# Optimization experiments

Hardware: AMD Instinct MI355X
Metric: run time of the kernel (lower is better)

## Reference

```python
import jax, jax.numpy as jnp
import numpy as np

NUM_BLOCKS = 2
NUM_LAYERS = 10
L = NUM_BLOCKS * NUM_LAYERS  # 20 wave layers
C_IN, C_RES, C_SKIP = 8, 64, 256
B, T = 32, 4096


def causal_conv1d(x, w, b, dilation=1):
    # x: [B, C_in, T], w: [C_out, C_in, K], left-pad so output is causal and length-preserving
    k = w.shape[2]
    out = jax.lax.conv_general_dilated(
        x, w, window_strides=(1,), padding=[(dilation * (k - 1), 0)],
        rhs_dilation=(dilation,), dimension_numbers=("NCH", "OIH", "NCH"))
    return out + b[None, :, None]


def setup_inputs() -> dict:
    key = jax.random.key(0)
    ks = jax.random.split(key, 12)
    s1 = 1.0 / np.sqrt(C_IN)
    s2 = 1.0 / np.sqrt(2 * C_RES)
    s3 = 1.0 / np.sqrt(C_RES)
    return {
        "x":    jax.random.normal(ks[0], (B, C_IN, T), jnp.float32),
        "w_in": jax.random.normal(ks[1], (C_RES, C_IN, 1), jnp.float32) * s1,
        "b_in": jax.random.normal(ks[2], (C_RES,), jnp.float32) * s1,
        "w_f":  jax.random.normal(ks[3], (L, C_RES, C_RES, 2), jnp.float32) * s2,
        "b_f":  jax.random.normal(ks[4], (L, C_RES), jnp.float32) * s2,
        "w_g":  jax.random.normal(ks[5], (L, C_RES, C_RES, 2), jnp.float32) * s2,
        "b_g":  jax.random.normal(ks[6], (L, C_RES), jnp.float32) * s2,
        "w_s":  jax.random.normal(ks[7], (L, C_SKIP, C_RES, 1), jnp.float32) * s3,
        "b_s":  jax.random.normal(ks[8], (L, C_SKIP), jnp.float32) * s3,
        "w_r":  jax.random.normal(ks[9], (L, C_RES, C_RES, 1), jnp.float32) * s3,
        "b_r":  jax.random.normal(ks[10], (L, C_RES), jnp.float32) * s3,
    }


def reference(x, w_in, b_in, w_f, b_f, w_g, b_g, w_s, b_s, w_r, b_r):
    # WaveNet.encode: 1x1 input conv, then num_blocks*num_layers gated dilated causal layers
    h = causal_conv1d(x, w_in, b_in)            # [B, C_RES, T]
    skips = jnp.zeros((x.shape[0], w_s.shape[1], x.shape[2]), x.dtype)
    for i in range(L):
        d = 2 ** (i % NUM_LAYERS)
        f = jnp.tanh(causal_conv1d(h, w_f[i], b_f[i], d))
        g = jax.nn.sigmoid(causal_conv1d(h, w_g[i], b_g[i], d))
        z = f * g                                # gated activation
        skips = skips + causal_conv1d(z, w_s[i], b_s[i])
        h = h + causal_conv1d(z, w_r[i], b_r[i])  # residual connection
    return skips
```

## Files before the change

### kernel.cpp

```cpp
#include <hip/hip_runtime.h>

#define B_ 32
#define T_ 4096
#define CR 64
#define CS 256
#define NL 20

typedef __bf16 bf16x8 __attribute__((ext_vector_type(8)));
typedef __bf16 bf16x4v __attribute__((ext_vector_type(4)));
typedef float f32x4 __attribute__((ext_vector_type(4)));

__device__ __forceinline__ f32x4 mfma16(bf16x8 a, bf16x8 b, f32x4 c) {
  return __builtin_amdgcn_mfma_f32_16x16x32_bf16(a, b, c, 0, 0, 0);
}

__global__ void pack_kernel(const float* __restrict__ wf, const float* __restrict__ wg,
                            const float* __restrict__ wsn, const float* __restrict__ wr,
                            const float* __restrict__ bs,
                            __bf16* __restrict__ Wfg2, __bf16* __restrict__ Wr2,
                            __bf16* __restrict__ Ws2, float* __restrict__ bsS) {
  int n = blockIdx.x * 256 + threadIdx.x;
  if (n < 327680) {
    int j = n & 7, lane = (n >> 3) & 63, fr = (n >> 9) & 7, mt = (n >> 12) & 3, i = n >> 14;
    int cs = mt * 16 + (lane & 15);
    int k = (fr & 3) * 32 + (lane >> 4) * 8 + j;
    int ci = k & 63, tap = k >> 6;
    const float* src = (fr < 4) ? wf : wg;
    Wfg2[n] = (__bf16)src[((i * 64 + cs) * 64 + ci) * 2 + tap];
  } else if (n < 409600) {
    int m = n - 327680;
    int j = m & 7, lane = (m >> 3) & 63, kc = (m >> 9) & 1, mt = (m >> 10) & 3, i = m >> 12;
    int cs = mt * 16 + (lane & 15);
    int ci = kc * 32 + (lane >> 4) * 8 + j;
    Wr2[m] = (__bf16)wr[(i * 64 + cs) * 64 + ci];
  } else if (n < 737280) {
    int m = n - 409600;
    int j = m & 7, lane = (m >> 3) & 63, kc = (m >> 9) & 1, tile = (m >> 10) & 15, i = m >> 14;
    int cs = tile * 16 + (lane & 15);
    int ci = kc * 32 + (lane >> 4) * 8 + j;
    Ws2[m] = (__bf16)wsn[i * 16384 + cs * 64 + ci];
  } else if (n < 737536) {
    int cs = n - 737280;
    float s = 0.f;
    for (int i = 0; i < NL; ++i) s += bs[i * 256 + cs];
    bsS[cs] = s;
  }
}

__global__ void inconv_kernel(const float* __restrict__ x, const float* __restrict__ w_in,
                              const float* __restrict__ b_in, float* __restrict__ h0) {
  __shared__ float w[64][8];
  __shared__ float bi[64];
  int tid = threadIdx.x;
  for (int k = tid; k < 512; k += 256) w[k >> 3][k & 7] = w_in[k];
  if (tid < 64) bi[tid] = b_in[tid];
  __syncthreads();
  int b = blockIdx.x >> 4;
  int t = ((blockIdx.x & 15) << 8) + tid;
  float xv[8];
#pragma unroll
  for (int ci = 0; ci < 8; ++ci) xv[ci] = x[((size_t)b * 8 + ci) * T_ + t];
  float* orow = h0 + ((size_t)b * T_ + t) * 64;
#pragma unroll
  for (int c0 = 0; c0 < 64; c0 += 4) {
    float s0 = bi[c0], s1 = bi[c0 + 1], s2 = bi[c0 + 2], s3 = bi[c0 + 3];
#pragma unroll
    for (int ci = 0; ci < 8; ++ci) {
      s0 += w[c0][ci] * xv[ci];
      s1 += w[c0 + 1][ci] * xv[ci];
      s2 += w[c0 + 2][ci] * xv[ci];
      s3 += w[c0 + 3][ci] * xv[ci];
    }
    float4 o = make_float4(s0, s1, s2, s3);
    *(float4*)(orow + c0) = o;
  }
}

__global__ __launch_bounds__(256) void layer_kernel(
    const float* __restrict__ h_in, float* __restrict__ h_out,
    const __bf16* __restrict__ Wfg, const __bf16* __restrict__ Wr,
    const float* __restrict__ bF, const float* __restrict__ bG,
    const float* __restrict__ bR,
    __bf16* __restrict__ Zg, int d, int il, int Gs) {
  __shared__ __bf16 sB[2][64][72];

  const int tid = threadIdx.x;
  const int bid = ((blockIdx.x & 7) << 8) | (blockIdx.x >> 3);
  const int b = bid >> 6;
  const int t0 = (bid & 63) << 6;
  const float* hbase = h_in + ((size_t)b * T_ + t0) * 64;

  float4 vc[4], vd[4];
#pragma unroll
  for (int it = 0; it < 4; ++it) {
    int f = (it * 256 + tid) * 4;
    int trr = f >> 6, c = f & 63;
    vc[it] = *(const float4*)(hbase + trr * 64 + c);
    int td = t0 + trr - d;
    vd[it] = make_float4(0.f, 0.f, 0.f, 0.f);
    if (td >= 0) vd[it] = *(const float4*)(h_in + ((size_t)b * T_ + td) * 64 + c);
  }
#pragma unroll
  for (int it = 0; it < 4; ++it) {
    int f = (it * 256 + tid) * 4;
    int trr = f >> 6, c = f & 63;
    bf16x4v pc = {(__bf16)vc[it].x, (__bf16)vc[it].y, (__bf16)vc[it].z, (__bf16)vc[it].w};
    *(bf16x4v*)&sB[1][trr][c] = pc;
    bf16x4v pd = {(__bf16)vd[it].x, (__bf16)vd[it].y, (__bf16)vd[it].z, (__bf16)vd[it].w};
    *(bf16x4v*)&sB[0][trr][c] = pd;
  }
  __syncthreads();

  const int lane = tid & 63, wid = tid >> 6;
  const int tl = (wid << 4) | (lane & 15);
  const int kq = lane >> 4;

  bf16x8 bh[4];
  bh[0] = *(const bf16x8*)&sB[0][tl][kq * 8];
  bh[1] = *(const bf16x8*)&sB[0][tl][32 + kq * 8];
  bh[2] = *(const bf16x8*)&sB[1][tl][kq * 8];
  bh[3] = *(const bf16x8*)&sB[1][tl][32 + kq * 8];

  __bf16 (*sZ)[72] = sB[0];
  __bf16* zrow = Zg + (((size_t)b * T_ + t0 + tl) * Gs + il) * 64;

#pragma unroll
  for (int mt = 0; mt < 4; ++mt) {
    const __bf16* wb = Wfg + (mt * 8) * 512 + lane * 8;
    f32x4 aF = {0.f, 0.f, 0.f, 0.f}, aG = {0.f, 0.f, 0.f, 0.f};
#pragma unroll
    for (int kc = 0; kc < 4; ++kc) {
      aF = mfma16(*(const bf16x8*)(wb + kc * 512), bh[kc], aF);
      aG = mfma16(*(const bf16x8*)(wb + (4 + kc) * 512), bh[kc], aG);
    }
    const int c0 = (mt << 4) + (kq << 2);
    float4 bfv = *(const float4*)(bF + c0);
    float4 bgv = *(const float4*)(bG + c0);
    float fb[4] = {bfv.x, bfv.y, bfv.z, bfv.w};
    float gb[4] = {bgv.x, bgv.y, bgv.z, bgv.w};
    bf16x4v zv;
#pragma unroll
    for (int r = 0; r < 4; ++r) {
      float fp = aF[r] + fb[r];
      float gp = aG[r] + gb[r];
      float e = __expf(2.f * fp);
      float th = 1.f - 2.f / (e + 1.f);
      float sg = 1.f / (1.f + __expf(-gp));
      zv[r] = (__bf16)(th * sg);
    }
    *(bf16x4v*)&sZ[tl][c0] = zv;
    *(bf16x4v*)(zrow + c0) = zv;
  }

  bf16x8 bz0 = *(const bf16x8*)&sZ[tl][kq * 8];
  bf16x8 bz1 = *(const bf16x8*)&sZ[tl][32 + kq * 8];
#pragma unroll
  for (int mt = 0; mt < 4; ++mt) {
    const __bf16* wrb = Wr + (mt * 2) * 512 + lane * 8;
    f32x4 aR = {0.f, 0.f, 0.f, 0.f};
    aR = mfma16(*(const bf16x8*)(wrb), bz0, aR);
    aR = mfma16(*(const bf16x8*)(wrb + 512), bz1, aR);
    const int c0 = (mt << 4) + (kq << 2);
    float4 hv = *(const float4*)(h_in + ((size_t)b * T_ + t0 + tl) * 64 + c0);
    float4 brv = *(const float4*)(bR + c0);
    float4 o;
    o.x = hv.x + aR[0] + brv.x;
    o.y = hv.y + aR[1] + brv.y;
    o.z = hv.z + aR[2] + brv.z;
    o.w = hv.w + aR[3] + brv.w;
    *(float4*)(h_out + ((size_t)b * T_ + t0 + tl) * 64 + c0) = o;
  }
}

__global__ __launch_bounds__(256) void skip_kernel(
    const __bf16* __restrict__ Zg, const __bf16* __restrict__ Ws2,
    const float* __restrict__ bsS, float* __restrict__ out,
    int i0, int cnt, int Gs, int first) {
  __shared__ __bf16 sZ[2][64][72];

  const int tid = threadIdx.x;
  const int b = blockIdx.x >> 6;
  const int t0 = (blockIdx.x & 63) << 6;
  const int lane = tid & 63, wid = tid >> 6;
  const int kq = lane >> 4;
  const int tr = tid >> 2, coff = (tid & 3) << 4;

  const __bf16* zbase = Zg + (((size_t)b * T_ + t0 + tr) * Gs) * 64 + coff;
  const __bf16* wbase = Ws2 + (size_t)i0 * 16384 + (size_t)(wid * 8) * 512 + lane * 8;

  uint4 a0 = *(const uint4*)zbase;
  uint4 a1 = *(const uint4*)(zbase + 8);
  bf16x8 aw[8];
#pragma unroll
  for (int f = 0; f < 8; ++f) aw[f] = *(const bf16x8*)(wbase + f * 512);
  uint4 p0 = {0, 0, 0, 0}, p1 = {0, 0, 0, 0};
  if (cnt > 1) {
    p0 = *(const uint4*)(zbase + 64);
    p1 = *(const uint4*)(zbase + 72);
  }
  *(uint4*)&sZ[0][tr][coff] = a0;
  *(uint4*)&sZ[0][tr][coff + 8] = a1;

  f32x4 acc[16];
#pragma unroll
  for (int q = 0; q < 16; ++q) acc[q] = (f32x4){0.f, 0.f, 0.f, 0.f};

  asm volatile("s_waitcnt lgkmcnt(0)" ::: "memory");
  __builtin_amdgcn_sched_barrier(0);
  __builtin_amdgcn_s_barrier();
  __builtin_amdgcn_sched_barrier(0);

  const char* zrow0 = (const char*)&sZ[0][0][0] + (lane & 15) * 144 + kq * 16;

  for (int il = 0; il < cnt; ++il) {
    const int cur = il & 1;
    const bool have1 = (il + 1) < cnt;
    const bool have2 = (il + 2) < cnt;

    bf16x8 awn[8];
    if (have1) {
#pragma unroll
      for (int f = 0; f < 8; ++f)
        awn[f] = *(const bf16x8*)(wbase + (size_t)(il + 1) * 16384 + f * 512);
    }
    uint4 q0, q1;
    if (have2) {
      q0 = *(const uint4*)(zbase + (size_t)(il + 2) * 64);
      q1 = *(const uint4*)(zbase + (size_t)(il + 2) * 64 + 8);
    }

    bf16x8 bz[8];
#pragma unroll
    for (int nt = 0; nt < 4; ++nt) {
      bz[nt * 2]     = *(const bf16x8*)(zrow0 + cur * 9216 + nt * 2304);
      bz[nt * 2 + 1] = *(const bf16x8*)(zrow0 + cur * 9216 + nt * 2304 + 64);
    }
#pragma unroll
    for (int mt = 0; mt < 4; ++mt) {
#pragma unroll
      for (int nt = 0; nt < 4; ++nt) {
        acc[mt * 4 + nt] = mfma16(aw[mt * 2], bz[nt * 2], acc[mt * 4 + nt]);
        acc[mt * 4 + nt] = mfma16(aw[mt * 2 + 1], bz[nt * 2 + 1], acc[mt * 4 + nt]);
      }
    }

    if (have1) {
      *(uint4*)&sZ[cur ^ 1][tr][coff] = p0;
      *(uint4*)&sZ[cur ^ 1][tr][coff + 8] = p1;
      if (have2) { p0 = q0; p1 = q1; }
#pragma unroll
      for (int f = 0; f < 8; ++f) aw[f] = awn[f];
      asm volatile("s_waitcnt lgkmcnt(0)" ::: "memory");
      __builtin_amdgcn_sched_barrier(0);
      __builtin_amdgcn_s_barrier();
      __builtin_amdgcn_sched_barrier(0);
    }
  }

  const int csb = wid * 64 + (kq << 2);
  const int tcol = t0 + (lane & 15);
#pragma unroll
  for (int mt = 0; mt < 4; ++mt) {
#pragma unroll
    for (int nt = 0; nt < 4; ++nt) {
#pragma unroll
      for (int r = 0; r < 4; ++r) {
        int cs = csb + mt * 16 + r;
        size_t idx = ((size_t)b * CS + cs) * T_ + tcol + nt * 16;
        float v = acc[mt * 4 + nt][r];
        if (first) out[idx] = v + bsS[cs];
        else out[idx] += v;
      }
    }
  }
}

extern "C" void kernel_launch(void* const* d_in, const int* in_sizes, int n_in,
                              void* d_out, int out_size, void* d_ws, size_t ws_size,
                              hipStream_t stream) {
  (void)in_sizes; (void)n_in; (void)out_size;
  const float* x    = (const float*)d_in[0];
  const float* w_in = (const float*)d_in[1];
  const float* b_in = (const float*)d_in[2];
  const float* w_f  = (const float*)d_in[3];
  const float* b_f  = (const float*)d_in[4];
  const float* w_g  = (const float*)d_in[5];
  const float* b_g  = (const float*)d_in[6];
  const float* w_s  = (const float*)d_in[7];
  const float* b_s  = (const float*)d_in[8];
  const float* w_r  = (const float*)d_in[9];
  const float* b_r  = (const float*)d_in[10];
  float* out = (float*)d_out;

  char* ws = (char*)d_ws;
  size_t off = 0;
  auto alloc = [&](size_t bytes) -> char* {
    char* p = ws + off;
    off = (off + bytes + 255) & ~(size_t)255;
    return p;
  };
  float* hA = (float*)alloc((size_t)B_ * T_ * 64 * 4);
  float* hB = (float*)alloc((size_t)B_ * T_ * 64 * 4);
  __bf16* Wfg2 = (__bf16*)alloc((size_t)NL * 16384 * 2);
  __bf16* Wr2  = (__bf16*)alloc((size_t)NL * 4096 * 2);
  __bf16* Ws2  = (__bf16*)alloc((size_t)NL * 16384 * 2);
  float* bsS = (float*)alloc(CS * 4);

  size_t zslot = (size_t)B_ * T_ * 64 * 2;
  size_t rem = (ws_size > off) ? (ws_size - off) : 0;
  int G = (int)(rem / zslot);
  if (G > NL) G = NL;
  if (G < 1) G = 1;
  __bf16* Zg = (__bf16*)(ws + off);

  hipLaunchKernelGGL(pack_kernel, dim3(2881), dim3(256), 0, stream,
                     w_f, w_g, w_s, w_r, b_s, Wfg2, Wr2, Ws2, bsS);
  hipLaunchKernelGGL(inconv_kernel, dim3(512), dim3(256), 0, stream, x, w_in, b_in, hA);

  float* hc = hA;
  float* hn = hB;
  int i0 = 0;
  for (int i = 0; i < NL; ++i) {
    int il = i - i0;
    hipLaunchKernelGGL(layer_kernel, dim3(B_ * 64), dim3(256), 0, stream,
                       hc, hn, Wfg2 + (size_t)i * 16384, Wr2 + (size_t)i * 4096,
                       b_f + i * 64, b_g + i * 64, b_r + i * 64,
                       Zg, 1 << (i % 10), il, G);
    { float* tmp = hc; hc = hn; hn = tmp; }
    if (il + 1 == G || i == NL - 1) {
      int cnt = il + 1;
      hipLaunchKernelGGL(skip_kernel, dim3(B_ * 64), dim3(256), 0, stream,
                         Zg, Ws2, bsS, out, i0, cnt, G, (i0 == 0) ? 1 : 0);
      i0 = i + 1;
    }
  }
}
```

Before: 1.011 ms.

## Store Z in MFMA-fragment tile layout and DMA it into LDS with triple buffering

The layer kernel now writes gated activations Z into per-block 4096-element tiles already arranged in MFMA B-fragment order, replacing row-major rows. The skip kernel loads these tiles with global_load_lds (direct global-to-LDS DMA) into a three-slot LDS ring two iterations ahead, and ping-pongs weight registers between awA and awB so no register copy is needed. LDS reads become contiguous lane*8 fragment loads with no padding. The aim is to remove the register-staged LDS stores and the waits on them, at the cost of hand-tuned vmcnt counts that must match the issued loads exactly.

```diff
diff --git a/kernel.cpp b/kernel.cpp
--- a/kernel.cpp
+++ b/kernel.cpp
@@ -12,6 +12,12 @@
 
 __device__ __forceinline__ f32x4 mfma16(bf16x8 a, bf16x8 b, f32x4 c) {
   return __builtin_amdgcn_mfma_f32_16x16x32_bf16(a, b, c, 0, 0, 0);
+}
+
+__device__ __forceinline__ void dma16(const __bf16* g, __bf16* l) {
+  __builtin_amdgcn_global_load_lds(
+      (const __attribute__((address_space(1))) unsigned int*)g,
+      (__attribute__((address_space(3))) unsigned int*)l, 16, 0, 0);
 }
 
 __global__ void pack_kernel(const float* __restrict__ wf, const float* __restrict__ wg,
@@ -122,7 +128,7 @@
   bh[3] = *(const bf16x8*)&sB[1][tl][32 + kq * 8];
 
   __bf16 (*sZ)[72] = sB[0];
-  __bf16* zrow = Zg + (((size_t)b * T_ + t0 + tl) * Gs + il) * 64;
+  __bf16* ztile = Zg + ((size_t)bid * Gs + il) * 4096;
 
 #pragma unroll
   for (int mt = 0; mt < 4; ++mt) {
@@ -149,7 +155,12 @@
       zv[r] = (__bf16)(th * sg);
     }
     *(bf16x4v*)&sZ[tl][c0] = zv;
-    *(bf16x4v*)(zrow + c0) = zv;
+    {
+      const int kc = mt >> 1;
+      const int l = ((mt & 1) * 2 + (kq >> 1)) * 16 + (lane & 15);
+      const int j0 = (kq & 1) * 4;
+      *(bf16x4v*)(ztile + (size_t)(wid * 2 + kc) * 512 + l * 8 + j0) = zv;
+    }
   }
 
   bf16x8 bz0 = *(const bf16x8*)&sZ[tl][kq * 8];
@@ -176,85 +187,95 @@
     const __bf16* __restrict__ Zg, const __bf16* __restrict__ Ws2,
     const float* __restrict__ bsS, float* __restrict__ out,
     int i0, int cnt, int Gs, int first) {
-  __shared__ __bf16 sZ[2][64][72];
+  __shared__ __bf16 sZ[3][4096];
 
   const int tid = threadIdx.x;
   const int b = blockIdx.x >> 6;
   const int t0 = (blockIdx.x & 63) << 6;
   const int lane = tid & 63, wid = tid >> 6;
   const int kq = lane >> 4;
-  const int tr = tid >> 2, coff = (tid & 3) << 4;
-
-  const __bf16* zbase = Zg + (((size_t)b * T_ + t0 + tr) * Gs) * 64 + coff;
+
+  const __bf16* ztile = Zg + ((size_t)blockIdx.x * Gs + i0) * 4096;
   const __bf16* wbase = Ws2 + (size_t)i0 * 16384 + (size_t)(wid * 8) * 512 + lane * 8;
-
-  uint4 a0 = *(const uint4*)zbase;
-  uint4 a1 = *(const uint4*)(zbase + 8);
-  bf16x8 aw[8];
-#pragma unroll
-  for (int f = 0; f < 8; ++f) aw[f] = *(const bf16x8*)(wbase + f * 512);
-  uint4 p0 = {0, 0, 0, 0}, p1 = {0, 0, 0, 0};
+  __bf16* ldsw = &sZ[0][0] + (size_t)(wid * 2) * 512;
+
+#define DMA_TILE(ilx, bufx)                                                   \
+  do {                                                                        \
+    const __bf16* gsrc_ = ztile + (size_t)(ilx) * 4096 + (wid * 2) * 512 + lane * 8; \
+    __bf16* ld_ = ldsw + (size_t)(bufx) * 4096;                               \
+    dma16(gsrc_, ld_);                                                        \
+    dma16(gsrc_ + 512, ld_ + 512);                                            \
+  } while (0)
+
+  f32x4 acc[16];
+#pragma unroll
+  for (int q = 0; q < 16; ++q) acc[q] = (f32x4){0.f, 0.f, 0.f, 0.f};
+
+  bf16x8 awA[8], awB[8];
+
+  DMA_TILE(0, 0);
+  __builtin_amdgcn_sched_barrier(0);
+#pragma unroll
+  for (int f = 0; f < 8; ++f) awA[f] = *(const bf16x8*)(wbase + f * 512);
+  __builtin_amdgcn_sched_barrier(0);
   if (cnt > 1) {
-    p0 = *(const uint4*)(zbase + 64);
-    p1 = *(const uint4*)(zbase + 72);
-  }
-  *(uint4*)&sZ[0][tr][coff] = a0;
-  *(uint4*)&sZ[0][tr][coff + 8] = a1;
-
-  f32x4 acc[16];
-#pragma unroll
-  for (int q = 0; q < 16; ++q) acc[q] = (f32x4){0.f, 0.f, 0.f, 0.f};
-
-  asm volatile("s_waitcnt lgkmcnt(0)" ::: "memory");
-  __builtin_amdgcn_sched_barrier(0);
+    DMA_TILE(1, 1);
+    __builtin_amdgcn_sched_barrier(0);
+    asm volatile("s_waitcnt vmcnt(10)" ::: "memory");
+  } else {
+    __builtin_amdgcn_sched_barrier(0);
+    asm volatile("s_waitcnt vmcnt(8)" ::: "memory");
+  }
   __builtin_amdgcn_s_barrier();
   __builtin_amdgcn_sched_barrier(0);
 
-  const char* zrow0 = (const char*)&sZ[0][0][0] + (lane & 15) * 144 + kq * 16;
-
-  for (int il = 0; il < cnt; ++il) {
-    const int cur = il & 1;
-    const bool have1 = (il + 1) < cnt;
-    const bool have2 = (il + 2) < cnt;
-
-    bf16x8 awn[8];
-    if (have1) {
-#pragma unroll
-      for (int f = 0; f < 8; ++f)
-        awn[f] = *(const bf16x8*)(wbase + (size_t)(il + 1) * 16384 + f * 512);
-    }
-    uint4 q0, q1;
-    if (have2) {
-      q0 = *(const uint4*)(zbase + (size_t)(il + 2) * 64);
-      q1 = *(const uint4*)(zbase + (size_t)(il + 2) * 64 + 8);
-    }
-
-    bf16x8 bz[8];
-#pragma unroll
-    for (int nt = 0; nt < 4; ++nt) {
-      bz[nt * 2]     = *(const bf16x8*)(zrow0 + cur * 9216 + nt * 2304);
-      bz[nt * 2 + 1] = *(const bf16x8*)(zrow0 + cur * 9216 + nt * 2304 + 64);
-    }
-#pragma unroll
-    for (int mt = 0; mt < 4; ++mt) {
-#pragma unroll
-      for (int nt = 0; nt < 4; ++nt) {
-        acc[mt * 4 + nt] = mfma16(aw[mt * 2], bz[nt * 2], acc[mt * 4 + nt]);
-        acc[mt * 4 + nt] = mfma16(aw[mt * 2 + 1], bz[nt * 2 + 1], acc[mt * 4 + nt]);
-      }
-    }
-
-    if (have1) {
-      *(uint4*)&sZ[cur ^ 1][tr][coff] = p0;
-      *(uint4*)&sZ[cur ^ 1][tr][coff + 8] = p1;
-      if (have2) { p0 = q0; p1 = q1; }
-#pragma unroll
-      for (int f = 0; f < 8; ++f) aw[f] = awn[f];
-      asm volatile("s_waitcnt lgkmcnt(0)" ::: "memory");
-      __builtin_amdgcn_sched_barrier(0);
-      __builtin_amdgcn_s_barrier();
-      __builtin_amdgcn_sched_barrier(0);
-    }
+#define SKIP_STEP(AWU, AWP)                                                   \
+  do {                                                                        \
+    const bool have1 = (il + 1) < cnt, have2 = (il + 2) < cnt;                \
+    if (have2) {                                                              \
+      int b2 = cur + 2;                                                       \
+      if (b2 >= 3) b2 -= 3;                                                   \
+      DMA_TILE(il + 2, b2);                                                   \
+    }                                                                         \
+    __builtin_amdgcn_sched_barrier(0);                                        \
+    if (have1) {                                                              \
+      const __bf16* wn_ = wbase + (size_t)(il + 1) * 16384;                   \
+      _Pragma("unroll") for (int f = 0; f < 8; ++f)                           \
+          AWP[f] = *(const bf16x8*)(wn_ + f * 512);                           \
+    }                                                                         \
+    const __bf16* zb_ = &sZ[0][0] + (size_t)cur * 4096 + lane * 8;            \
+    bf16x8 bz[4];                                                             \
+    _Pragma("unroll") for (int f = 0; f < 4; ++f)                             \
+        bz[f] = *(const bf16x8*)(zb_ + f * 512);                              \
+    _Pragma("unroll") for (int mt = 0; mt < 4; ++mt)                          \
+        _Pragma("unroll") for (int nt = 0; nt < 2; ++nt) {                    \
+      acc[mt * 4 + nt] = mfma16(AWU[mt * 2], bz[nt * 2], acc[mt * 4 + nt]);   \
+      acc[mt * 4 + nt] = mfma16(AWU[mt * 2 + 1], bz[nt * 2 + 1], acc[mt * 4 + nt]); \
+    }                                                                         \
+    _Pragma("unroll") for (int f = 0; f < 4; ++f)                             \
+        bz[f] = *(const bf16x8*)(zb_ + (4 + f) * 512);                        \
+    _Pragma("unroll") for (int mt = 0; mt < 4; ++mt)                          \
+        _Pragma("unroll") for (int nt = 0; nt < 2; ++nt) {                    \
+      acc[mt * 4 + nt + 2] = mfma16(AWU[mt * 2], bz[nt * 2], acc[mt * 4 + nt + 2]); \
+      acc[mt * 4 + nt + 2] =                                                  \
+          mfma16(AWU[mt * 2 + 1], bz[nt * 2 + 1], acc[mt * 4 + nt + 2]);      \
+    }                                                                         \
+    if (have1) {                                                              \
+      __builtin_amdgcn_sched_barrier(0);                                      \
+      asm volatile("s_waitcnt vmcnt(10) lgkmcnt(0)" ::: "memory");            \
+      __builtin_amdgcn_s_barrier();                                           \
+      __builtin_amdgcn_sched_barrier(0);                                      \
+    }                                                                         \
+  } while (0)
+
+  int il = 0, cur = 0;
+  while (true) {
+    SKIP_STEP(awA, awB);
+    if (++il == cnt) break;
+    cur = (cur == 2) ? 0 : cur + 1;
+    SKIP_STEP(awB, awA);
+    if (++il == cnt) break;
+    cur = (cur == 2) ? 0 : cur + 1;
   }
 
   const int csb = wid * 64 + (kq << 2);
```

Result: faster. 954.2 us (-5.6%).

## Store gated Z in MFMA-fragment layout and drop LDS staging in skip kernel

Applied to the files above, without the earlier changes.

The layer kernel now writes the gated activation Z to global memory in a pre-swizzled per-tile layout that matches the MFMA B-operand fragment order. This lets the skip kernel load its operands straight from global into registers, removing the LDS double buffer and its barriers. The skip kernel also splits each 64-step time tile into two 32-step halves, doubling the grid and halving accumulators per thread. The trade-off is that weights are reloaded by twice as many blocks and there is no explicit prefetch pipelining any more.

```diff
diff --git a/kernel.cpp b/kernel.cpp
--- a/kernel.cpp
+++ b/kernel.cpp
@@ -122,7 +122,7 @@
   bh[3] = *(const bf16x8*)&sB[1][tl][32 + kq * 8];
 
   __bf16 (*sZ)[72] = sB[0];
-  __bf16* zrow = Zg + (((size_t)b * T_ + t0 + tl) * Gs + il) * 64;
+  __bf16* ztile = Zg + ((size_t)bid * Gs + il) * 4096;
 
 #pragma unroll
   for (int mt = 0; mt < 4; ++mt) {
@@ -149,7 +149,12 @@
       zv[r] = (__bf16)(th * sg);
     }
     *(bf16x4v*)&sZ[tl][c0] = zv;
-    *(bf16x4v*)(zrow + c0) = zv;
+    {
+      const int kc = mt >> 1;
+      const int l = ((mt & 1) * 2 + (kq >> 1)) * 16 + (lane & 15);
+      const int j0 = (kq & 1) * 4;
+      *(bf16x4v*)(ztile + (size_t)(wid * 2 + kc) * 512 + l * 8 + j0) = zv;
+    }
   }
 
   bf16x8 bz0 = *(const bf16x8*)&sZ[tl][kq * 8];
@@ -176,84 +181,39 @@
     const __bf16* __restrict__ Zg, const __bf16* __restrict__ Ws2,
     const float* __restrict__ bsS, float* __restrict__ out,
     int i0, int cnt, int Gs, int first) {
-  __shared__ __bf16 sZ[2][64][72];
-
   const int tid = threadIdx.x;
-  const int b = blockIdx.x >> 6;
-  const int t0 = (blockIdx.x & 63) << 6;
+  const int bx = blockIdx.x;
+  const int b = bx >> 7;
+  const int t64 = (bx >> 1) & 63;
+  const int h = bx & 1;
+  const int t0 = (t64 << 6) + (h << 5);
   const int lane = tid & 63, wid = tid >> 6;
   const int kq = lane >> 4;
-  const int tr = tid >> 2, coff = (tid & 3) << 4;
-
-  const __bf16* zbase = Zg + (((size_t)b * T_ + t0 + tr) * Gs) * 64 + coff;
-  const __bf16* wbase = Ws2 + (size_t)i0 * 16384 + (size_t)(wid * 8) * 512 + lane * 8;
-
-  uint4 a0 = *(const uint4*)zbase;
-  uint4 a1 = *(const uint4*)(zbase + 8);
-  bf16x8 aw[8];
-#pragma unroll
-  for (int f = 0; f < 8; ++f) aw[f] = *(const bf16x8*)(wbase + f * 512);
-  uint4 p0 = {0, 0, 0, 0}, p1 = {0, 0, 0, 0};
-  if (cnt > 1) {
-    p0 = *(const uint4*)(zbase + 64);
-    p1 = *(const uint4*)(zbase + 72);
-  }
-  *(uint4*)&sZ[0][tr][coff] = a0;
-  *(uint4*)&sZ[0][tr][coff + 8] = a1;
-
-  f32x4 acc[16];
-#pragma unroll
-  for (int q = 0; q < 16; ++q) acc[q] = (f32x4){0.f, 0.f, 0.f, 0.f};
-
-  asm volatile("s_waitcnt lgkmcnt(0)" ::: "memory");
-  __builtin_amdgcn_sched_barrier(0);
-  __builtin_amdgcn_s_barrier();
-  __builtin_amdgcn_sched_barrier(0);
-
-  const char* zrow0 = (const char*)&sZ[0][0][0] + (lane & 15) * 144 + kq * 16;
-
+
+  const __bf16* zb = Zg + ((size_t)(b * 64 + t64) * Gs + i0) * 4096 + h * 2048 + lane * 8;
+  const __bf16* wb = Ws2 + (size_t)i0 * 16384 + (size_t)(wid * 8) * 512 + lane * 8;
+
+  f32x4 acc[8];
+#pragma unroll
+  for (int q = 0; q < 8; ++q) acc[q] = (f32x4){0.f, 0.f, 0.f, 0.f};
+
+#pragma unroll 2
   for (int il = 0; il < cnt; ++il) {
-    const int cur = il & 1;
-    const bool have1 = (il + 1) < cnt;
-    const bool have2 = (il + 2) < cnt;
-
-    bf16x8 awn[8];
-    if (have1) {
-#pragma unroll
-      for (int f = 0; f < 8; ++f)
-        awn[f] = *(const bf16x8*)(wbase + (size_t)(il + 1) * 16384 + f * 512);
-    }
-    uint4 q0, q1;
-    if (have2) {
-      q0 = *(const uint4*)(zbase + (size_t)(il + 2) * 64);
-      q1 = *(const uint4*)(zbase + (size_t)(il + 2) * 64 + 8);
-    }
-
-    bf16x8 bz[8];
-#pragma unroll
-    for (int nt = 0; nt < 4; ++nt) {
-      bz[nt * 2]     = *(const bf16x8*)(zrow0 + cur * 9216 + nt * 2304);
-      bz[nt * 2 + 1] = *(const bf16x8*)(zrow0 + cur * 9216 + nt * 2304 + 64);
-    }
+    bf16x8 bz[4];
+    bf16x8 aw[8];
+#pragma unroll
+    for (int f = 0; f < 4; ++f)
+      bz[f] = *(const bf16x8*)(zb + (size_t)il * 4096 + f * 512);
+#pragma unroll
+    for (int f = 0; f < 8; ++f)
+      aw[f] = *(const bf16x8*)(wb + (size_t)il * 16384 + f * 512);
 #pragma unroll
     for (int mt = 0; mt < 4; ++mt) {
 #pragma unroll
-      for (int nt = 0; nt < 4; ++nt) {
-        acc[mt * 4 + nt] = mfma16(aw[mt * 2], bz[nt * 2], acc[mt * 4 + nt]);
-        acc[mt * 4 + nt] = mfma16(aw[mt * 2 + 1], bz[nt * 2 + 1], acc[mt * 4 + nt]);
+      for (int nt = 0; nt < 2; ++nt) {
+        acc[mt * 2 + nt] = mfma16(aw[mt * 2], bz[nt * 2], acc[mt * 2 + nt]);
+        acc[mt * 2 + nt] = mfma16(aw[mt * 2 + 1], bz[nt * 2 + 1], acc[mt * 2 + nt]);
       }
-    }
-
-    if (have1) {
-      *(uint4*)&sZ[cur ^ 1][tr][coff] = p0;
-      *(uint4*)&sZ[cur ^ 1][tr][coff + 8] = p1;
-      if (have2) { p0 = q0; p1 = q1; }
-#pragma unroll
-      for (int f = 0; f < 8; ++f) aw[f] = awn[f];
-      asm volatile("s_waitcnt lgkmcnt(0)" ::: "memory");
-      __builtin_amdgcn_sched_barrier(0);
-      __builtin_amdgcn_s_barrier();
-      __builtin_amdgcn_sched_barrier(0);
     }
   }
 
@@ -262,12 +222,12 @@
 #pragma unroll
   for (int mt = 0; mt < 4; ++mt) {
 #pragma unroll
-    for (int nt = 0; nt < 4; ++nt) {
+    for (int nt = 0; nt < 2; ++nt) {
 #pragma unroll
       for (int r = 0; r < 4; ++r) {
         int cs = csb + mt * 16 + r;
         size_t idx = ((size_t)b * CS + cs) * T_ + tcol + nt * 16;
-        float v = acc[mt * 4 + nt][r];
+        float v = acc[mt * 2 + nt][r];
         if (first) out[idx] = v + bsS[cs];
         else out[idx] += v;
       }
@@ -329,7 +289,7 @@
     { float* tmp = hc; hc = hn; hn = tmp; }
     if (il + 1 == G || i == NL - 1) {
       int cnt = il + 1;
-      hipLaunchKernelGGL(skip_kernel, dim3(B_ * 64), dim3(256), 0, stream,
+      hipLaunchKernelGGL(skip_kernel, dim3(B_ * 128), dim3(256), 0, stream,
                          Zg, Ws2, bsS, out, i0, cnt, G, (i0 == 0) ? 1 : 0);
       i0 = i + 1;
     }
```

Result: slower. 1.049 ms (+3.7%).
